# Kernel tuning notes

Hardware: AMD Instinct MI355X
Metric: run time of the kernel (lower is better)

The kernel has to match this reference:

```python
import jax, jax.numpy as jnp
import numpy as np

N = 50000
E = 800000
IN = 128
HID = 64
HEADS = 4
OUT = 128
NEG_SLOPE = 0.2


def _segment_softmax(logits, seg, num_segments):
    # logits: (E, H), seg: (E,) destination node ids
    m = jax.ops.segment_max(logits, seg, num_segments=num_segments)
    m = jnp.where(jnp.isfinite(m), m, 0.0)
    e = jnp.exp(logits - m[seg])
    s = jax.ops.segment_sum(e, seg, num_segments=num_segments)
    return e / (s[seg] + 1e-16)


def _gat_conv(x, edge_index, W, att_src, att_dst, bias, heads, out_ch, concat):
    # PyG GATConv with add_self_loops=True, negative_slope=0.2 (eval mode: no dropout)
    n = x.shape[0]
    loops = jnp.arange(n, dtype=edge_index.dtype)
    src = jnp.concatenate([edge_index[0], loops])
    dst = jnp.concatenate([edge_index[1], loops])
    h = (x @ W).reshape(n, heads, out_ch)                      # (N, H, C)
    a_src = jnp.einsum('nhc,hc->nh', h, att_src)               # (N, H)
    a_dst = jnp.einsum('nhc,hc->nh', h, att_dst)
    logits = jax.nn.leaky_relu(a_src[src] + a_dst[dst], NEG_SLOPE)  # (E', H)
    alpha = _segment_softmax(logits, dst, n)                   # (E', H)
    msg = alpha[:, :, None] * h[src]                           # (E', H, C)
    out = jax.ops.segment_sum(msg, dst, num_segments=n)        # (N, H, C)
    if concat:
        out = out.reshape(n, heads * out_ch)
    else:
        out = out.mean(axis=1)
    return out + bias


def setup_inputs() -> dict:
    key = jax.random.key(0)
    ks = jax.random.split(key, 16)
    hc = HID * HEADS
    s = 0.1
    return {
        'x': jax.random.normal(ks[0], (N, IN), dtype=jnp.float32),
        'edge_index': jax.random.randint(ks[1], (2, E), 0, N, dtype=jnp.int64),
        'W1': jax.random.normal(ks[2], (IN, hc), dtype=jnp.float32) * s,
        'att_src1': jax.random.normal(ks[3], (HEADS, HID), dtype=jnp.float32) * s,
        'att_dst1': jax.random.normal(ks[4], (HEADS, HID), dtype=jnp.float32) * s,
        'b1': jnp.zeros((hc,), dtype=jnp.float32),
        'lin1_w': jax.random.normal(ks[5], (IN, hc), dtype=jnp.float32) * s,
        'lin1_b': jnp.zeros((hc,), dtype=jnp.float32),
        'W2': jax.random.normal(ks[6], (hc, OUT), dtype=jnp.float32) * s,
        'att_src2': jax.random.normal(ks[7], (1, OUT), dtype=jnp.float32) * s,
        'att_dst2': jax.random.normal(ks[8], (1, OUT), dtype=jnp.float32) * s,
        'b2': jnp.zeros((OUT,), dtype=jnp.float32),
        'lin2_w': jax.random.normal(ks[9], (hc, OUT), dtype=jnp.float32) * s,
        'lin2_b': jnp.zeros((OUT,), dtype=jnp.float32),
    }


def reference(x, edge_index, W1, att_src1, att_dst1, b1, lin1_w, lin1_b,
              W2, att_src2, att_dst2, b2, lin2_w, lin2_b):
    # h1 = ELU(GATConv1(x) + Linear1(x))  (dropout is eval-mode no-op)
    h = _gat_conv(x, edge_index, W1, att_src1, att_dst1, b1, HEADS, HID, True)
    h = jax.nn.elu(h + x @ lin1_w + lin1_b)
    # out = GATConv2(h) + Linear2(h)
    o = _gat_conv(h, edge_index, W2, att_src2, att_dst2, b2, 1, OUT, False)
    return o + h @ lin2_w + lin2_b
```

## Files before the change

kernel.cpp:

```cpp
#include <hip/hip_runtime.h>
#include <math.h>

#define N_NODES 50000
#define N_EDGES 800000
#define EP (N_EDGES + N_NODES)
#define IN_CH 128
#define HID 64
#define HEADS 4
#define HC (HID * HEADS)
#define OUT_CH 128
#define NEG_SLOPE 0.2f
#define NSCAN ((N_NODES + 255) / 256)
#define MTILES (N_NODES / 16)

typedef __bf16 bf16x8 __attribute__((ext_vector_type(8)));
typedef float  f32x4  __attribute__((ext_vector_type(4)));

__device__ __forceinline__ float bf2f(unsigned short u) {
    return __uint_as_float(((unsigned)u) << 16);
}
__device__ __forceinline__ unsigned short f2bf(float f) {
    unsigned u = __float_as_uint(f);
    return (unsigned short)((u + 0x7fffu + ((u >> 16) & 1u)) >> 16);
}
__device__ __forceinline__ float lrelu(float v) {
    return v > 0.f ? v : NEG_SLOPE * v;
}
__device__ __forceinline__ bf16x8 ldfrag(const unsigned short* p) {
    uint4 u = *(const uint4*)p;
    return __builtin_bit_cast(bf16x8, u);
}

__global__ void hist_kernel(const int* __restrict__ ei, int* __restrict__ cnt) {
    int e = blockIdx.x * 256 + threadIdx.x;
    if (e >= EP) return;
    int d = (e < N_EDGES) ? ei[N_EDGES + e] : e - N_EDGES;
    atomicAdd(&cnt[d], 1);
}

__global__ void scan1_kernel(const int* __restrict__ cnt,
                             int* __restrict__ row, int* __restrict__ bsum) {
    __shared__ int buf[256];
    int i = blockIdx.x * 256 + threadIdx.x;
    int v = (i < N_NODES) ? cnt[i] : 0;
    buf[threadIdx.x] = v;
    __syncthreads();
#pragma unroll
    for (int off = 1; off < 256; off <<= 1) {
        int t = (threadIdx.x >= off) ? buf[threadIdx.x - off] : 0;
        __syncthreads();
        buf[threadIdx.x] += t;
        __syncthreads();
    }
    if (i < N_NODES) row[i] = buf[threadIdx.x] - v;
    if (threadIdx.x == 255) bsum[blockIdx.x] = buf[255];
}

__global__ void scan2_kernel(const int* __restrict__ bsum,
                             int* __restrict__ boff, int* __restrict__ rowN) {
    __shared__ int buf[256];
    int tid = threadIdx.x;
    int v = (tid < NSCAN) ? bsum[tid] : 0;
    buf[tid] = v;
    __syncthreads();
#pragma unroll
    for (int off = 1; off < 256; off <<= 1) {
        int t = (tid >= off) ? buf[tid - off] : 0;
        __syncthreads();
        buf[tid] += t;
        __syncthreads();
    }
    if (tid < NSCAN) boff[tid] = buf[tid] - v;
    if (tid == 255) rowN[0] = buf[255];
}

__global__ void scan3_kernel(int* __restrict__ row, const int* __restrict__ boff,
                             int* __restrict__ pos) {
    int i = blockIdx.x * 256 + threadIdx.x;
    if (i >= N_NODES) return;
    int r = row[i] + boff[blockIdx.x];
    row[i] = r;
    pos[i] = r;
}

__global__ void scatter_kernel(const int* __restrict__ ei,
                               int* __restrict__ pos,
                               int* __restrict__ adjS, int* __restrict__ adjD) {
    int e = blockIdx.x * 256 + threadIdx.x;
    if (e >= EP) return;
    int s, d;
    if (e < N_EDGES) { s = ei[e]; d = ei[N_EDGES + e]; }
    else             { s = d = e - N_EDGES; }
    int p = atomicAdd(&pos[d], 1);
    adjS[p] = s;
    adjD[p] = d;
}

__global__ void convx_kernel(const float* __restrict__ x,
                             unsigned short* __restrict__ xb) {
    int i = blockIdx.x * 256 + threadIdx.x;
    if (i >= N_NODES * (IN_CH / 4)) return;
    float4 v = ((const float4*)x)[i];
    ushort4 o;
    o.x = f2bf(v.x); o.y = f2bf(v.y); o.z = f2bf(v.z); o.w = f2bf(v.w);
    ((ushort4*)xb)[i] = o;
}

__global__ void pack1_kernel(const float* __restrict__ W1,
                             const float* __restrict__ L1,
                             unsigned short* __restrict__ Bp) {
    int t = blockIdx.x * 256 + threadIdx.x;
    if (t >= 128 * 64) return;
    int frag = t >> 6, l = t & 63;
    int ks = frag >> 5, nf = frag & 31;
    int col = nf * 16 + (l & 15);
    int kb = ks * 32 + (l >> 4) * 8;
    unsigned short* o = Bp + (size_t)t * 8;
#pragma unroll
    for (int i = 0; i < 8; ++i) {
        int k = kb + i;
        float v = (col < HC) ? W1[k * HC + col] : L1[k * HC + (col - HC)];
        o[i] = f2bf(v);
    }
}

__global__ void pack2_kernel(const float* __restrict__ W2,
                             const float* __restrict__ L2,
                             unsigned short* __restrict__ Bp) {
    int t = blockIdx.x * 256 + threadIdx.x;
    if (t >= 128 * 64) return;
    int frag = t >> 6, l = t & 63;
    int ks = frag >> 4, nf = frag & 15;
    int col = nf * 16 + (l & 15);
    int kb = ks * 32 + (l >> 4) * 8;
    unsigned short* o = Bp + (size_t)t * 8;
#pragma unroll
    for (int i = 0; i < 8; ++i) {
        int k = kb + i;
        float v = (col < OUT_CH) ? W2[k * OUT_CH + col]
                                 : L2[k * OUT_CH + (col - OUT_CH)];
        o[i] = f2bf(v);
    }
}

__global__ __launch_bounds__(256) void gemm1_mfma(
        const unsigned short* __restrict__ xb,
        const unsigned short* __restrict__ Bp,
        unsigned short* __restrict__ H1b, float* __restrict__ XL1) {
    int m0 = blockIdx.x * 16;
    int w = threadIdx.x >> 6, l = threadIdx.x & 63;
    int row = m0 + (l & 15);
    int koff = (l >> 4) * 8;
    f32x4 acc[8];
#pragma unroll
    for (int f = 0; f < 8; ++f) acc[f] = (f32x4){0.f, 0.f, 0.f, 0.f};
#pragma unroll
    for (int ks = 0; ks < 4; ++ks) {
        bf16x8 a = ldfrag(xb + (size_t)row * IN_CH + ks * 32 + koff);
        const unsigned short* bb = Bp + ((size_t)((ks * 32 + w * 8) * 64 + l)) * 8;
#pragma unroll
        for (int f = 0; f < 8; ++f) {
            bf16x8 b = ldfrag(bb + (size_t)f * 512);
            acc[f] = __builtin_amdgcn_mfma_f32_16x16x32_bf16(a, b, acc[f], 0, 0, 0);
        }
    }
    int rq = (l >> 4) * 4, lc = l & 15;
#pragma unroll
    for (int f = 0; f < 8; ++f) {
        int col = w * 128 + f * 16 + lc;
#pragma unroll
        for (int r = 0; r < 4; ++r) {
            int m = m0 + rq + r;
            float v = acc[f][r];
            if (col < HC) H1b[(size_t)m * HC + col] = f2bf(v);
            else          XL1[(size_t)m * HC + (col - HC)] = v;
        }
    }
}

__global__ __launch_bounds__(256) void gemm2_mfma(
        const unsigned short* __restrict__ HBb,
        const unsigned short* __restrict__ Bp,
        unsigned short* __restrict__ H2b, float* __restrict__ XL2) {
    int m0 = blockIdx.x * 16;
    int w = threadIdx.x >> 6, l = threadIdx.x & 63;
    int row = m0 + (l & 15);
    int koff = (l >> 4) * 8;
    f32x4 acc[4];
#pragma unroll
    for (int f = 0; f < 4; ++f) acc[f] = (f32x4){0.f, 0.f, 0.f, 0.f};
#pragma unroll
    for (int ks = 0; ks < 8; ++ks) {
        bf16x8 a = ldfrag(HBb + (size_t)row * HC + ks * 32 + koff);
        const unsigned short* bb = Bp + ((size_t)((ks * 16 + w * 4) * 64 + l)) * 8;
#pragma unroll
        for (int f = 0; f < 4; ++f) {
            bf16x8 b = ldfrag(bb + (size_t)f * 512);
            acc[f] = __builtin_amdgcn_mfma_f32_16x16x32_bf16(a, b, acc[f], 0, 0, 0);
        }
    }
    int rq = (l >> 4) * 4, lc = l & 15;
#pragma unroll
    for (int f = 0; f < 4; ++f) {
        int col = w * 64 + f * 16 + lc;
#pragma unroll
        for (int r = 0; r < 4; ++r) {
            int m = m0 + rq + r;
            float v = acc[f][r];
            if (col < OUT_CH) H2b[(size_t)m * OUT_CH + col] = f2bf(v);
            else              XL2[(size_t)m * OUT_CH + (col - OUT_CH)] = v;
        }
    }
}

__global__ void att1_kernel(const unsigned short* __restrict__ H1b,
                            const float* __restrict__ as,
                            const float* __restrict__ ad,
                            float* __restrict__ AS, float* __restrict__ AD) {
    int n = blockIdx.x * 4 + (threadIdx.x >> 6);
    int l = threadIdx.x & 63;
    if (n >= N_NODES) return;
    const unsigned short* h = H1b + (size_t)n * HC;
    float vs[HEADS], vd[HEADS];
#pragma unroll
    for (int hh = 0; hh < HEADS; ++hh) {
        float v = bf2f(h[hh * HID + l]);
        vs[hh] = v * as[hh * HID + l];
        vd[hh] = v * ad[hh * HID + l];
    }
#pragma unroll
    for (int off = 32; off; off >>= 1)
#pragma unroll
        for (int hh = 0; hh < HEADS; ++hh) {
            vs[hh] += __shfl_down(vs[hh], off, 64);
            vd[hh] += __shfl_down(vd[hh], off, 64);
        }
    if (l == 0)
#pragma unroll
        for (int hh = 0; hh < HEADS; ++hh) {
            AS[n * HEADS + hh] = vs[hh];
            AD[n * HEADS + hh] = vd[hh];
        }
}

__global__ void att2_kernel(const unsigned short* __restrict__ H2b,
                            const float* __restrict__ as2,
                            const float* __restrict__ ad2,
                            float* __restrict__ AS, float* __restrict__ AD) {
    int n = blockIdx.x * 4 + (threadIdx.x >> 6);
    int l = threadIdx.x & 63;
    if (n >= N_NODES) return;
    const unsigned short* h = H2b + (size_t)n * OUT_CH;
    float v0 = bf2f(h[l]), v1 = bf2f(h[64 + l]);
    float vs = v0 * as2[l] + v1 * as2[64 + l];
    float vd = v0 * ad2[l] + v1 * ad2[64 + l];
#pragma unroll
    for (int off = 32; off; off >>= 1) {
        vs += __shfl_down(vs, off, 64);
        vd += __shfl_down(vd, off, 64);
    }
    if (l == 0) { AS[n] = vs; AD[n] = vd; }
}

__global__ void el1_kernel(const int* __restrict__ adjS,
                           const int* __restrict__ adjD,
                           const float* __restrict__ AS,
                           const float* __restrict__ AD,
                           float* __restrict__ EL) {
    int idx = blockIdx.x * 256 + threadIdx.x;
    if (idx >= HEADS * EP) return;
    int h = idx / EP, p = idx - h * EP;
    int s = adjS[p], d = adjD[p];
    EL[idx] = expf(lrelu(AS[s * HEADS + h] + AD[d * HEADS + h]));
}

__global__ void el2_kernel(const int* __restrict__ adjS,
                           const int* __restrict__ adjD,
                           const float* __restrict__ AS,
                           const float* __restrict__ AD,
                           float* __restrict__ EL) {
    int p = blockIdx.x * 256 + threadIdx.x;
    if (p >= EP) return;
    EL[p] = expf(lrelu(AS[adjS[p]] + AD[adjD[p]]));
}

__global__ void gather1_kernel(const int* __restrict__ row,
                               const int* __restrict__ adjS,
                               const float* __restrict__ EL,
                               const unsigned short* __restrict__ H1b,
                               const float* __restrict__ XL1,
                               const float* __restrict__ b1,
                               const float* __restrict__ l1b,
                               unsigned short* __restrict__ HBb) {
    int d = blockIdx.x, j = threadIdx.x;
    int hh = j >> 4;
    int beg = row[d], end = row[d + 1];
    const float* ELh = EL + (size_t)hh * EP;
    const ushort4* Hr = (const ushort4*)H1b;
    float a0 = 0.f, a1 = 0.f, a2 = 0.f, a3 = 0.f, esum = 0.f;
    int i = beg;
    for (; i + 4 <= end; i += 4) {
        int s0 = adjS[i], s1 = adjS[i + 1], s2 = adjS[i + 2], s3 = adjS[i + 3];
        float e0 = ELh[i], e1 = ELh[i + 1], e2 = ELh[i + 2], e3 = ELh[i + 3];
        ushort4 q0 = Hr[(size_t)s0 * 64 + j];
        ushort4 q1 = Hr[(size_t)s1 * 64 + j];
        ushort4 q2 = Hr[(size_t)s2 * 64 + j];
        ushort4 q3 = Hr[(size_t)s3 * 64 + j];
        a0 += e0 * bf2f(q0.x) + e1 * bf2f(q1.x) + e2 * bf2f(q2.x) + e3 * bf2f(q3.x);
        a1 += e0 * bf2f(q0.y) + e1 * bf2f(q1.y) + e2 * bf2f(q2.y) + e3 * bf2f(q3.y);
        a2 += e0 * bf2f(q0.z) + e1 * bf2f(q1.z) + e2 * bf2f(q2.z) + e3 * bf2f(q3.z);
        a3 += e0 * bf2f(q0.w) + e1 * bf2f(q1.w) + e2 * bf2f(q2.w) + e3 * bf2f(q3.w);
        esum += e0 + e1 + e2 + e3;
    }
    for (; i < end; ++i) {
        int s = adjS[i];
        float e = ELh[i];
        ushort4 q = Hr[(size_t)s * 64 + j];
        a0 += e * bf2f(q.x); a1 += e * bf2f(q.y);
        a2 += e * bf2f(q.z); a3 += e * bf2f(q.w);
        esum += e;
    }
    float inv = 1.f / (esum + 1e-16f);
    float4 xl = ((const float4*)XL1)[(size_t)d * 64 + j];
    float4 bb = ((const float4*)b1)[j];
    float4 lb = ((const float4*)l1b)[j];
    float v0 = a0 * inv + xl.x + bb.x + lb.x;
    float v1 = a1 * inv + xl.y + bb.y + lb.y;
    float v2 = a2 * inv + xl.z + bb.z + lb.z;
    float v3 = a3 * inv + xl.w + bb.w + lb.w;
    v0 = v0 > 0.f ? v0 : expm1f(v0);
    v1 = v1 > 0.f ? v1 : expm1f(v1);
    v2 = v2 > 0.f ? v2 : expm1f(v2);
    v3 = v3 > 0.f ? v3 : expm1f(v3);
    ushort4 o;
    o.x = f2bf(v0); o.y = f2bf(v1); o.z = f2bf(v2); o.w = f2bf(v3);
    ((ushort4*)HBb)[(size_t)d * 64 + j] = o;
}

__global__ void gather2_kernel(const int* __restrict__ row,
                               const int* __restrict__ adjS,
                               const float* __restrict__ EL,
                               const unsigned short* __restrict__ H2b,
                               const float* __restrict__ XL2,
                               const float* __restrict__ b2,
                               const float* __restrict__ l2b,
                               float* __restrict__ out) {
    int d = blockIdx.x, l = threadIdx.x;
    int beg = row[d], end = row[d + 1];
    const ushort2* Hr = (const ushort2*)H2b;
    float ax = 0.f, ay = 0.f, esum = 0.f;
    int i = beg;
    for (; i + 4 <= end; i += 4) {
        int s0 = adjS[i], s1 = adjS[i + 1], s2 = adjS[i + 2], s3 = adjS[i + 3];
        float e0 = EL[i], e1 = EL[i + 1], e2 = EL[i + 2], e3 = EL[i + 3];
        ushort2 q0 = Hr[(size_t)s0 * 64 + l];
        ushort2 q1 = Hr[(size_t)s1 * 64 + l];
        ushort2 q2 = Hr[(size_t)s2 * 64 + l];
        ushort2 q3 = Hr[(size_t)s3 * 64 + l];
        ax += e0 * bf2f(q0.x) + e1 * bf2f(q1.x) + e2 * bf2f(q2.x) + e3 * bf2f(q3.x);
        ay += e0 * bf2f(q0.y) + e1 * bf2f(q1.y) + e2 * bf2f(q2.y) + e3 * bf2f(q3.y);
        esum += e0 + e1 + e2 + e3;
    }
    for (; i < end; ++i) {
        int s = adjS[i];
        float e = EL[i];
        ushort2 q = Hr[(size_t)s * 64 + l];
        ax += e * bf2f(q.x); ay += e * bf2f(q.y);
        esum += e;
    }
    float inv = 1.f / (esum + 1e-16f);
    float2 xl = ((const float2*)XL2)[(size_t)d * 64 + l];
    float2 bb = ((const float2*)b2)[l];
    float2 lb = ((const float2*)l2b)[l];
    ((float2*)out)[(size_t)d * 64 + l] =
        make_float2(ax * inv + xl.x + bb.x + lb.x,
                    ay * inv + xl.y + bb.y + lb.y);
}

extern "C" void kernel_launch(void* const* d_in, const int* in_sizes, int n_in,
                              void* d_out, int out_size, void* d_ws, size_t ws_size,
                              hipStream_t stream) {
    const float* x    = (const float*)d_in[0];
    const int*   ei   = (const int*)d_in[1];
    const float* W1   = (const float*)d_in[2];
    const float* as1  = (const float*)d_in[3];
    const float* ad1  = (const float*)d_in[4];
    const float* b1   = (const float*)d_in[5];
    const float* l1w  = (const float*)d_in[6];
    const float* l1b  = (const float*)d_in[7];
    const float* W2   = (const float*)d_in[8];
    const float* as2  = (const float*)d_in[9];
    const float* ad2  = (const float*)d_in[10];
    const float* b2   = (const float*)d_in[11];
    const float* l2w  = (const float*)d_in[12];
    const float* l2b  = (const float*)d_in[13];
    float* out = (float*)d_out;

    float* ws = (float*)d_ws;
    unsigned short* xb  = (unsigned short*)ws;
    float* fp = ws + (size_t)N_NODES * 64;
    unsigned short* H1b = (unsigned short*)fp;
    fp += (size_t)N_NODES * 128;
    float* XL1 = fp;
    fp += (size_t)N_NODES * HC;
    unsigned short* HBb = (unsigned short*)fp;
    fp += (size_t)N_NODES * 128;
    float* AS1 = fp; fp += (size_t)N_NODES * HEADS;
    float* AD1 = fp; fp += (size_t)N_NODES * HEADS;
    float* AS2 = fp; fp += N_NODES;
    float* AD2 = fp; fp += N_NODES;
    float* EL1 = fp; fp += (size_t)HEADS * EP;
    unsigned short* Bp1 = (unsigned short*)fp; fp += 32768;
    unsigned short* Bp2 = (unsigned short*)fp; fp += 32768;
    int* cnt  = (int*)fp;
    int* row  = cnt + N_NODES;
    int* pos  = row + N_NODES + 1;
    int* bsum = pos + N_NODES;
    int* boff = bsum + NSCAN;
    int* adjS = boff + NSCAN;
    int* adjD = adjS + EP;
    unsigned short* H2b = H1b;
    float* XL2 = XL1;
    float* EL2 = EL1;

    int nE = (EP + 255) / 256;

    hipMemsetAsync(cnt, 0, N_NODES * 4, stream);
    hist_kernel<<<nE, 256, 0, stream>>>(ei, cnt);
    scan1_kernel<<<NSCAN, 256, 0, stream>>>(cnt, row, bsum);
    scan2_kernel<<<1, 256, 0, stream>>>(bsum, boff, row + N_NODES);
    scan3_kernel<<<NSCAN, 256, 0, stream>>>(row, boff, pos);
    scatter_kernel<<<nE, 256, 0, stream>>>(ei, pos, adjS, adjD);

    convx_kernel<<<(N_NODES * (IN_CH / 4) + 255) / 256, 256, 0, stream>>>(x, xb);
    pack1_kernel<<<(128 * 64 + 255) / 256, 256, 0, stream>>>(W1, l1w, Bp1);
    pack2_kernel<<<(128 * 64 + 255) / 256, 256, 0, stream>>>(W2, l2w, Bp2);

    gemm1_mfma<<<MTILES, 256, 0, stream>>>(xb, Bp1, H1b, XL1);
    att1_kernel<<<(N_NODES + 3) / 4, 256, 0, stream>>>(H1b, as1, ad1, AS1, AD1);
    el1_kernel<<<(HEADS * EP + 255) / 256, 256, 0, stream>>>(adjS, adjD, AS1, AD1, EL1);
    gather1_kernel<<<N_NODES, 64, 0, stream>>>(row, adjS, EL1, H1b, XL1,
                                               b1, l1b, HBb);

    gemm2_mfma<<<MTILES, 256, 0, stream>>>(HBb, Bp2, H2b, XL2);
    att2_kernel<<<(N_NODES + 3) / 4, 256, 0, stream>>>(H2b, as2, ad2, AS2, AD2);
    el2_kernel<<<nE, 256, 0, stream>>>(adjS, adjD, AS2, AD2, EL2);
    gather2_kernel<<<N_NODES, 64, 0, stream>>>(row, adjS, EL2, H2b, XL2,
                                               b2, l2b, out);
}
```

Before: 333.9 us.

## Fuse attention scores into GEMMs, merge edge-logit with CSR scatter, bf16 skip path

Attention-score dot products are now computed in the MFMA GEMM epilogues, which removes the separate att1/att2 kernels and their re-read of H. Layer-1 edge exponentials are computed inside the CSR scatter kernel and stored as float4 per edge position, replacing the el1 kernel and its head-major array. The two weight-pack kernels are merged into one. The linear skip outputs are stored as bf16 instead of fp32. The gather loops are unrolled to 8 edges with loads batched ahead of use. Together these cut kernel launches and memory traffic, but the skip path loses precision and the scatter kernel now does more work.

```diff
diff --git a/kernel.cpp b/kernel.cpp
--- a/kernel.cpp
+++ b/kernel.cpp
@@ -83,9 +83,12 @@
     pos[i] = r;
 }
 
-__global__ void scatter_kernel(const int* __restrict__ ei,
-                               int* __restrict__ pos,
-                               int* __restrict__ adjS, int* __restrict__ adjD) {
+__global__ void scatter_el1_kernel(const int* __restrict__ ei,
+                                   int* __restrict__ pos,
+                                   const float4* __restrict__ AS4,
+                                   const float4* __restrict__ AD4,
+                                   int* __restrict__ adjS, int* __restrict__ adjD,
+                                   float4* __restrict__ EL4) {
     int e = blockIdx.x * 256 + threadIdx.x;
     if (e >= EP) return;
     int s, d;
@@ -94,6 +97,13 @@
     int p = atomicAdd(&pos[d], 1);
     adjS[p] = s;
     adjD[p] = d;
+    float4 a = AS4[s], b = AD4[d];
+    float4 o;
+    o.x = expf(lrelu(a.x + b.x));
+    o.y = expf(lrelu(a.y + b.y));
+    o.z = expf(lrelu(a.z + b.z));
+    o.w = expf(lrelu(a.w + b.w));
+    EL4[p] = o;
 }
 
 __global__ void convx_kernel(const float* __restrict__ x,
@@ -106,57 +116,59 @@
     ((ushort4*)xb)[i] = o;
 }
 
-__global__ void pack1_kernel(const float* __restrict__ W1,
-                             const float* __restrict__ L1,
-                             unsigned short* __restrict__ Bp) {
+__global__ void pack12_kernel(const float* __restrict__ W1,
+                              const float* __restrict__ L1,
+                              const float* __restrict__ W2,
+                              const float* __restrict__ L2,
+                              unsigned short* __restrict__ Bp1,
+                              unsigned short* __restrict__ Bp2) {
     int t = blockIdx.x * 256 + threadIdx.x;
-    if (t >= 128 * 64) return;
-    int frag = t >> 6, l = t & 63;
-    int ks = frag >> 5, nf = frag & 31;
-    int col = nf * 16 + (l & 15);
-    int kb = ks * 32 + (l >> 4) * 8;
-    unsigned short* o = Bp + (size_t)t * 8;
-#pragma unroll
-    for (int i = 0; i < 8; ++i) {
-        int k = kb + i;
-        float v = (col < HC) ? W1[k * HC + col] : L1[k * HC + (col - HC)];
-        o[i] = f2bf(v);
-    }
-}
-
-__global__ void pack2_kernel(const float* __restrict__ W2,
-                             const float* __restrict__ L2,
-                             unsigned short* __restrict__ Bp) {
-    int t = blockIdx.x * 256 + threadIdx.x;
-    if (t >= 128 * 64) return;
-    int frag = t >> 6, l = t & 63;
-    int ks = frag >> 4, nf = frag & 15;
-    int col = nf * 16 + (l & 15);
-    int kb = ks * 32 + (l >> 4) * 8;
-    unsigned short* o = Bp + (size_t)t * 8;
-#pragma unroll
-    for (int i = 0; i < 8; ++i) {
-        int k = kb + i;
-        float v = (col < OUT_CH) ? W2[k * OUT_CH + col]
-                                 : L2[k * OUT_CH + (col - OUT_CH)];
-        o[i] = f2bf(v);
+    if (t < 8192) {
+        int frag = t >> 6, l = t & 63;
+        int ks = frag >> 5, nf = frag & 31;
+        int col = nf * 16 + (l & 15);
+        int kb = ks * 32 + (l >> 4) * 8;
+        unsigned short* o = Bp1 + (size_t)t * 8;
+#pragma unroll
+        for (int i = 0; i < 8; ++i) {
+            int k = kb + i;
+            float v = (col < HC) ? W1[k * HC + col] : L1[k * HC + (col - HC)];
+            o[i] = f2bf(v);
+        }
+    } else if (t < 16384) {
+        int u = t - 8192;
+        int frag = u >> 6, l = u & 63;
+        int ks = frag >> 4, nf = frag & 15;
+        int col = nf * 16 + (l & 15);
+        int kb = ks * 32 + (l >> 4) * 8;
+        unsigned short* o = Bp2 + (size_t)u * 8;
+#pragma unroll
+        for (int i = 0; i < 8; ++i) {
+            int k = kb + i;
+            float v = (col < OUT_CH) ? W2[k * OUT_CH + col]
+                                     : L2[k * OUT_CH + (col - OUT_CH)];
+            o[i] = f2bf(v);
+        }
     }
 }
 
 __global__ __launch_bounds__(256) void gemm1_mfma(
         const unsigned short* __restrict__ xb,
         const unsigned short* __restrict__ Bp,
-        unsigned short* __restrict__ H1b, float* __restrict__ XL1) {
+        const float* __restrict__ as1, const float* __restrict__ ad1,
+        unsigned short* __restrict__ H1b, unsigned short* __restrict__ XLb,
+        float* __restrict__ AS, float* __restrict__ AD) {
+    __shared__ float sAS[16][4], sAD[16][4];
     int m0 = blockIdx.x * 16;
     int w = threadIdx.x >> 6, l = threadIdx.x & 63;
-    int row = m0 + (l & 15);
+    int arow = m0 + (l & 15);
     int koff = (l >> 4) * 8;
     f32x4 acc[8];
 #pragma unroll
     for (int f = 0; f < 8; ++f) acc[f] = (f32x4){0.f, 0.f, 0.f, 0.f};
 #pragma unroll
     for (int ks = 0; ks < 4; ++ks) {
-        bf16x8 a = ldfrag(xb + (size_t)row * IN_CH + ks * 32 + koff);
+        bf16x8 a = ldfrag(xb + (size_t)arow * IN_CH + ks * 32 + koff);
         const unsigned short* bb = Bp + ((size_t)((ks * 32 + w * 8) * 64 + l)) * 8;
 #pragma unroll
         for (int f = 0; f < 8; ++f) {
@@ -164,34 +176,75 @@
             acc[f] = __builtin_amdgcn_mfma_f32_16x16x32_bf16(a, b, acc[f], 0, 0, 0);
         }
     }
-    int rq = (l >> 4) * 4, lc = l & 15;
+    int g = l >> 4, lc = l & 15;
 #pragma unroll
     for (int f = 0; f < 8; ++f) {
         int col = w * 128 + f * 16 + lc;
 #pragma unroll
         for (int r = 0; r < 4; ++r) {
-            int m = m0 + rq + r;
+            int m = m0 + g * 4 + r;
             float v = acc[f][r];
             if (col < HC) H1b[(size_t)m * HC + col] = f2bf(v);
-            else          XL1[(size_t)m * HC + (col - HC)] = v;
-        }
-    }
+            else          XLb[(size_t)m * HC + (col - HC)] = f2bf(v);
+        }
+    }
+    if (w < 2) {
+        float ps[4][2], pd[4][2];
+#pragma unroll
+        for (int r = 0; r < 4; ++r) { ps[r][0]=ps[r][1]=pd[r][0]=pd[r][1]=0.f; }
+#pragma unroll
+        for (int f = 0; f < 8; ++f) {
+            int col = w * 128 + f * 16 + lc;
+            float av = as1[col], dv = ad1[col];
+            int hp = f >> 2;
+#pragma unroll
+            for (int r = 0; r < 4; ++r) {
+                ps[r][hp] += acc[f][r] * av;
+                pd[r][hp] += acc[f][r] * dv;
+            }
+        }
+#pragma unroll
+        for (int msk = 1; msk < 16; msk <<= 1)
+#pragma unroll
+            for (int r = 0; r < 4; ++r) {
+                ps[r][0] += __shfl_xor(ps[r][0], msk, 64);
+                ps[r][1] += __shfl_xor(ps[r][1], msk, 64);
+                pd[r][0] += __shfl_xor(pd[r][0], msk, 64);
+                pd[r][1] += __shfl_xor(pd[r][1], msk, 64);
+            }
+        if (lc == 0)
+#pragma unroll
+            for (int r = 0; r < 4; ++r) {
+                sAS[g * 4 + r][w * 2 + 0] = ps[r][0];
+                sAS[g * 4 + r][w * 2 + 1] = ps[r][1];
+                sAD[g * 4 + r][w * 2 + 0] = pd[r][0];
+                sAD[g * 4 + r][w * 2 + 1] = pd[r][1];
+            }
+    }
+    __syncthreads();
+    int t = threadIdx.x;
+    if (t < 64)       AS[(m0 + (t >> 2)) * 4 + (t & 3)] = sAS[t >> 2][t & 3];
+    else if (t < 128) { int u = t - 64;
+                        AD[(m0 + (u >> 2)) * 4 + (u & 3)] = sAD[u >> 2][u & 3]; }
 }
 
 __global__ __launch_bounds__(256) void gemm2_mfma(
         const unsigned short* __restrict__ HBb,
         const unsigned short* __restrict__ Bp,
-        unsigned short* __restrict__ H2b, float* __restrict__ XL2) {
+        const float* __restrict__ as2, const float* __restrict__ ad2,
+        unsigned short* __restrict__ H2b, unsigned short* __restrict__ XLb,
+        float* __restrict__ AS, float* __restrict__ AD) {
+    __shared__ float sAS[16][2], sAD[16][2];
     int m0 = blockIdx.x * 16;
     int w = threadIdx.x >> 6, l = threadIdx.x & 63;
-    int row = m0 + (l & 15);
+    int arow = m0 + (l & 15);
     int koff = (l >> 4) * 8;
     f32x4 acc[4];
 #pragma unroll
     for (int f = 0; f < 4; ++f) acc[f] = (f32x4){0.f, 0.f, 0.f, 0.f};
 #pragma unroll
     for (int ks = 0; ks < 8; ++ks) {
-        bf16x8 a = ldfrag(HBb + (size_t)row * HC + ks * 32 + koff);
+        bf16x8 a = ldfrag(HBb + (size_t)arow * HC + ks * 32 + koff);
         const unsigned short* bb = Bp + ((size_t)((ks * 16 + w * 4) * 64 + l)) * 8;
 #pragma unroll
         for (int f = 0; f < 4; ++f) {
@@ -199,79 +252,50 @@
             acc[f] = __builtin_amdgcn_mfma_f32_16x16x32_bf16(a, b, acc[f], 0, 0, 0);
         }
     }
-    int rq = (l >> 4) * 4, lc = l & 15;
+    int g = l >> 4, lc = l & 15;
 #pragma unroll
     for (int f = 0; f < 4; ++f) {
         int col = w * 64 + f * 16 + lc;
 #pragma unroll
         for (int r = 0; r < 4; ++r) {
-            int m = m0 + rq + r;
+            int m = m0 + g * 4 + r;
             float v = acc[f][r];
             if (col < OUT_CH) H2b[(size_t)m * OUT_CH + col] = f2bf(v);
-            else              XL2[(size_t)m * OUT_CH + (col - OUT_CH)] = v;
-        }
-    }
-}
-
-__global__ void att1_kernel(const unsigned short* __restrict__ H1b,
-                            const float* __restrict__ as,
-                            const float* __restrict__ ad,
-                            float* __restrict__ AS, float* __restrict__ AD) {
-    int n = blockIdx.x * 4 + (threadIdx.x >> 6);
-    int l = threadIdx.x & 63;
-    if (n >= N_NODES) return;
-    const unsigned short* h = H1b + (size_t)n * HC;
-    float vs[HEADS], vd[HEADS];
-#pragma unroll
-    for (int hh = 0; hh < HEADS; ++hh) {
-        float v = bf2f(h[hh * HID + l]);
-        vs[hh] = v * as[hh * HID + l];
-        vd[hh] = v * ad[hh * HID + l];
-    }
-#pragma unroll
-    for (int off = 32; off; off >>= 1)
-#pragma unroll
-        for (int hh = 0; hh < HEADS; ++hh) {
-            vs[hh] += __shfl_down(vs[hh], off, 64);
-            vd[hh] += __shfl_down(vd[hh], off, 64);
-        }
-    if (l == 0)
-#pragma unroll
-        for (int hh = 0; hh < HEADS; ++hh) {
-            AS[n * HEADS + hh] = vs[hh];
-            AD[n * HEADS + hh] = vd[hh];
-        }
-}
-
-__global__ void att2_kernel(const unsigned short* __restrict__ H2b,
-                            const float* __restrict__ as2,
-                            const float* __restrict__ ad2,
-                            float* __restrict__ AS, float* __restrict__ AD) {
-    int n = blockIdx.x * 4 + (threadIdx.x >> 6);
-    int l = threadIdx.x & 63;
-    if (n >= N_NODES) return;
-    const unsigned short* h = H2b + (size_t)n * OUT_CH;
-    float v0 = bf2f(h[l]), v1 = bf2f(h[64 + l]);
-    float vs = v0 * as2[l] + v1 * as2[64 + l];
-    float vd = v0 * ad2[l] + v1 * ad2[64 + l];
-#pragma unroll
-    for (int off = 32; off; off >>= 1) {
-        vs += __shfl_down(vs, off, 64);
-        vd += __shfl_down(vd, off, 64);
-    }
-    if (l == 0) { AS[n] = vs; AD[n] = vd; }
-}
-
-__global__ void el1_kernel(const int* __restrict__ adjS,
-                           const int* __restrict__ adjD,
-                           const float* __restrict__ AS,
-                           const float* __restrict__ AD,
-                           float* __restrict__ EL) {
-    int idx = blockIdx.x * 256 + threadIdx.x;
-    if (idx >= HEADS * EP) return;
-    int h = idx / EP, p = idx - h * EP;
-    int s = adjS[p], d = adjD[p];
-    EL[idx] = expf(lrelu(AS[s * HEADS + h] + AD[d * HEADS + h]));
+            else              XLb[(size_t)m * OUT_CH + (col - OUT_CH)] = f2bf(v);
+        }
+    }
+    if (w < 2) {
+        float ps[4], pd[4];
+#pragma unroll
+        for (int r = 0; r < 4; ++r) { ps[r] = 0.f; pd[r] = 0.f; }
+#pragma unroll
+        for (int f = 0; f < 4; ++f) {
+            int col = w * 64 + f * 16 + lc;
+            float av = as2[col], dv = ad2[col];
+#pragma unroll
+            for (int r = 0; r < 4; ++r) {
+                ps[r] += acc[f][r] * av;
+                pd[r] += acc[f][r] * dv;
+            }
+        }
+#pragma unroll
+        for (int msk = 1; msk < 16; msk <<= 1)
+#pragma unroll
+            for (int r = 0; r < 4; ++r) {
+                ps[r] += __shfl_xor(ps[r], msk, 64);
+                pd[r] += __shfl_xor(pd[r], msk, 64);
+            }
+        if (lc == 0)
+#pragma unroll
+            for (int r = 0; r < 4; ++r) {
+                sAS[g * 4 + r][w] = ps[r];
+                sAD[g * 4 + r][w] = pd[r];
+            }
+    }
+    __syncthreads();
+    int t = threadIdx.x;
+    if (t < 16)       AS[m0 + t] = sAS[t][0] + sAS[t][1];
+    else if (t < 32)  { int u = t - 16; AD[m0 + u] = sAD[u][0] + sAD[u][1]; }
 }
 
 __global__ void el2_kernel(const int* __restrict__ adjS,
@@ -286,48 +310,53 @@
 
 __global__ void gather1_kernel(const int* __restrict__ row,
                                const int* __restrict__ adjS,
-                               const float* __restrict__ EL,
+                               const float4* __restrict__ EL4,
                                const unsigned short* __restrict__ H1b,
-                               const float* __restrict__ XL1,
+                               const unsigned short* __restrict__ XLb,
                                const float* __restrict__ b1,
                                const float* __restrict__ l1b,
                                unsigned short* __restrict__ HBb) {
     int d = blockIdx.x, j = threadIdx.x;
     int hh = j >> 4;
     int beg = row[d], end = row[d + 1];
-    const float* ELh = EL + (size_t)hh * EP;
     const ushort4* Hr = (const ushort4*)H1b;
     float a0 = 0.f, a1 = 0.f, a2 = 0.f, a3 = 0.f, esum = 0.f;
     int i = beg;
-    for (; i + 4 <= end; i += 4) {
-        int s0 = adjS[i], s1 = adjS[i + 1], s2 = adjS[i + 2], s3 = adjS[i + 3];
-        float e0 = ELh[i], e1 = ELh[i + 1], e2 = ELh[i + 2], e3 = ELh[i + 3];
-        ushort4 q0 = Hr[(size_t)s0 * 64 + j];
-        ushort4 q1 = Hr[(size_t)s1 * 64 + j];
-        ushort4 q2 = Hr[(size_t)s2 * 64 + j];
-        ushort4 q3 = Hr[(size_t)s3 * 64 + j];
-        a0 += e0 * bf2f(q0.x) + e1 * bf2f(q1.x) + e2 * bf2f(q2.x) + e3 * bf2f(q3.x);
-        a1 += e0 * bf2f(q0.y) + e1 * bf2f(q1.y) + e2 * bf2f(q2.y) + e3 * bf2f(q3.y);
-        a2 += e0 * bf2f(q0.z) + e1 * bf2f(q1.z) + e2 * bf2f(q2.z) + e3 * bf2f(q3.z);
-        a3 += e0 * bf2f(q0.w) + e1 * bf2f(q1.w) + e2 * bf2f(q2.w) + e3 * bf2f(q3.w);
-        esum += e0 + e1 + e2 + e3;
+    for (; i + 8 <= end; i += 8) {
+        int sa[8]; float ea[8]; ushort4 qa[8];
+#pragma unroll
+        for (int k = 0; k < 8; ++k) sa[k] = adjS[i + k];
+#pragma unroll
+        for (int k = 0; k < 8; ++k) {
+            float4 t = EL4[i + k];
+            ea[k] = hh < 2 ? (hh == 0 ? t.x : t.y) : (hh == 2 ? t.z : t.w);
+        }
+#pragma unroll
+        for (int k = 0; k < 8; ++k) qa[k] = Hr[(size_t)sa[k] * 64 + j];
+#pragma unroll
+        for (int k = 0; k < 8; ++k) {
+            a0 += ea[k] * bf2f(qa[k].x); a1 += ea[k] * bf2f(qa[k].y);
+            a2 += ea[k] * bf2f(qa[k].z); a3 += ea[k] * bf2f(qa[k].w);
+            esum += ea[k];
+        }
     }
     for (; i < end; ++i) {
         int s = adjS[i];
-        float e = ELh[i];
+        float4 t = EL4[i];
+        float e = hh < 2 ? (hh == 0 ? t.x : t.y) : (hh == 2 ? t.z : t.w);
         ushort4 q = Hr[(size_t)s * 64 + j];
         a0 += e * bf2f(q.x); a1 += e * bf2f(q.y);
         a2 += e * bf2f(q.z); a3 += e * bf2f(q.w);
         esum += e;
     }
     float inv = 1.f / (esum + 1e-16f);
-    float4 xl = ((const float4*)XL1)[(size_t)d * 64 + j];
+    ushort4 xq = ((const ushort4*)XLb)[(size_t)d * 64 + j];
     float4 bb = ((const float4*)b1)[j];
     float4 lb = ((const float4*)l1b)[j];
-    float v0 = a0 * inv + xl.x + bb.x + lb.x;
-    float v1 = a1 * inv + xl.y + bb.y + lb.y;
-    float v2 = a2 * inv + xl.z + bb.z + lb.z;
-    float v3 = a3 * inv + xl.w + bb.w + lb.w;
+    float v0 = a0 * inv + bf2f(xq.x) + bb.x + lb.x;
+    float v1 = a1 * inv + bf2f(xq.y) + bb.y + lb.y;
+    float v2 = a2 * inv + bf2f(xq.z) + bb.z + lb.z;
+    float v3 = a3 * inv + bf2f(xq.w) + bb.w + lb.w;
     v0 = v0 > 0.f ? v0 : expm1f(v0);
     v1 = v1 > 0.f ? v1 : expm1f(v1);
     v2 = v2 > 0.f ? v2 : expm1f(v2);
@@ -341,7 +370,7 @@
                                const int* __restrict__ adjS,
                                const float* __restrict__ EL,
                                const unsigned short* __restrict__ H2b,
-                               const float* __restrict__ XL2,
+                               const unsigned short* __restrict__ XLb,
                                const float* __restrict__ b2,
                                const float* __restrict__ l2b,
                                float* __restrict__ out) {
@@ -350,16 +379,20 @@
     const ushort2* Hr = (const ushort2*)H2b;
     float ax = 0.f, ay = 0.f, esum = 0.f;
     int i = beg;
-    for (; i + 4 <= end; i += 4) {
-        int s0 = adjS[i], s1 = adjS[i + 1], s2 = adjS[i + 2], s3 = adjS[i + 3];
-        float e0 = EL[i], e1 = EL[i + 1], e2 = EL[i + 2], e3 = EL[i + 3];
-        ushort2 q0 = Hr[(size_t)s0 * 64 + l];
-        ushort2 q1 = Hr[(size_t)s1 * 64 + l];
-        ushort2 q2 = Hr[(size_t)s2 * 64 + l];
-        ushort2 q3 = Hr[(size_t)s3 * 64 + l];
-        ax += e0 * bf2f(q0.x) + e1 * bf2f(q1.x) + e2 * bf2f(q2.x) + e3 * bf2f(q3.x);
-        ay += e0 * bf2f(q0.y) + e1 * bf2f(q1.y) + e2 * bf2f(q2.y) + e3 * bf2f(q3.y);
-        esum += e0 + e1 + e2 + e3;
+    for (; i + 8 <= end; i += 8) {
+        int sa[8]; float ea[8]; ushort2 qa[8];
+#pragma unroll
+        for (int k = 0; k < 8; ++k) sa[k] = adjS[i + k];
+#pragma unroll
+        for (int k = 0; k < 8; ++k) ea[k] = EL[i + k];
+#pragma unroll
+        for (int k = 0; k < 8; ++k) qa[k] = Hr[(size_t)sa[k] * 64 + l];
+#pragma unroll
+        for (int k = 0; k < 8; ++k) {
+            ax += ea[k] * bf2f(qa[k].x);
+            ay += ea[k] * bf2f(qa[k].y);
+            esum += ea[k];
+        }
     }
     for (; i < end; ++i) {
         int s = adjS[i];
@@ -369,12 +402,12 @@
         esum += e;
     }
     float inv = 1.f / (esum + 1e-16f);
-    float2 xl = ((const float2*)XL2)[(size_t)d * 64 + l];
+    ushort2 xq = ((const ushort2*)XLb)[(size_t)d * 64 + l];
     float2 bb = ((const float2*)b2)[l];
     float2 lb = ((const float2*)l2b)[l];
     ((float2*)out)[(size_t)d * 64 + l] =
-        make_float2(ax * inv + xl.x + bb.x + lb.x,
-                    ay * inv + xl.y + bb.y + lb.y);
+        make_float2(ax * inv + bf2f(xq.x) + bb.x + lb.x,
+                    ay * inv + bf2f(xq.y) + bb.y + lb.y);
 }
 
 extern "C" void kernel_launch(void* const* d_in, const int* in_sizes, int n_in,
@@ -401,15 +434,15 @@
     float* fp = ws + (size_t)N_NODES * 64;
     unsigned short* H1b = (unsigned short*)fp;
     fp += (size_t)N_NODES * 128;
-    float* XL1 = fp;
-    fp += (size_t)N_NODES * HC;
+    unsigned short* XLb = (unsigned short*)fp;
+    fp += (size_t)N_NODES * 128;
     unsigned short* HBb = (unsigned short*)fp;
     fp += (size_t)N_NODES * 128;
     float* AS1 = fp; fp += (size_t)N_NODES * HEADS;
     float* AD1 = fp; fp += (size_t)N_NODES * HEADS;
     float* AS2 = fp; fp += N_NODES;
     float* AD2 = fp; fp += N_NODES;
-    float* EL1 = fp; fp += (size_t)HEADS * EP;
+    float* EL1 = fp; fp += (size_t)EP * 4;
     unsigned short* Bp1 = (unsigned short*)fp; fp += 32768;
     unsigned short* Bp2 = (unsigned short*)fp; fp += 32768;
     int* cnt  = (int*)fp;
@@ -420,7 +453,7 @@
     int* adjS = boff + NSCAN;
     int* adjD = adjS + EP;
     unsigned short* H2b = H1b;
-    float* XL2 = XL1;
+    unsigned short* XL2b = XLb;
     float* EL2 = EL1;
 
     int nE = (EP + 255) / 256;
@@ -430,21 +463,19 @@
     scan1_kernel<<<NSCAN, 256, 0, stream>>>(cnt, row, bsum);
     scan2_kernel<<<1, 256, 0, stream>>>(bsum, boff, row + N_NODES);
     scan3_kernel<<<NSCAN, 256, 0, stream>>>(row, boff, pos);
-    scatter_kernel<<<nE, 256, 0, stream>>>(ei, pos, adjS, adjD);
 
     convx_kernel<<<(N_NODES * (IN_CH / 4) + 255) / 256, 256, 0, stream>>>(x, xb);
-    pack1_kernel<<<(128 * 64 + 255) / 256, 256, 0, stream>>>(W1, l1w, Bp1);
-    pack2_kernel<<<(128 * 64 + 255) / 256, 256, 0, stream>>>(W2, l2w, Bp2);
-
-    gemm1_mfma<<<MTILES, 256, 0, stream>>>(xb, Bp1, H1b, XL1);
-    att1_kernel<<<(N_NODES + 3) / 4, 256, 0, stream>>>(H1b, as1, ad1, AS1, AD1);
-    el1_kernel<<<(HEADS * EP + 255) / 256, 256, 0, stream>>>(adjS, adjD, AS1, AD1, EL1);
-    gather1_kernel<<<N_NODES, 64, 0, stream>>>(row, adjS, EL1, H1b, XL1,
-                                               b1, l1b, HBb);
-
-    gemm2_mfma<<<MTILES, 256, 0, stream>>>(HBb, Bp2, H2b, XL2);
-    att2_kernel<<<(N_NODES + 3) / 4, 256, 0, stream>>>(H2b, as2, ad2, AS2, AD2);
+    pack12_kernel<<<64, 256, 0, stream>>>(W1, l1w, W2, l2w, Bp1, Bp2);
+
+    gemm1_mfma<<<MTILES, 256, 0, stream>>>(xb, Bp1, as1, ad1, H1b, XLb, AS1, AD1);
+    scatter_el1_kernel<<<nE, 256, 0, stream>>>(ei, pos, (const float4*)AS1,
+                                               (const float4*)AD1, adjS, adjD,
+                                               (float4*)EL1);
+    gather1_kernel<<<N_NODES, 64, 0, stream>>>(row, adjS, (const float4*)EL1,
+                                               H1b, XLb, b1, l1b, HBb);
+
+    gemm2_mfma<<<MTILES, 256, 0, stream>>>(HBb, Bp2, as2, ad2, H2b, XL2b, AS2, AD2);
     el2_kernel<<<nE, 256, 0, stream>>>(adjS, adjD, AS2, AD2, EL2);
-    gather2_kernel<<<N_NODES, 64, 0, stream>>>(row, adjS, EL2, H2b, XL2,
+    gather2_kernel<<<N_NODES, 64, 0, stream>>>(row, adjS, EL2, H2b, XL2b,
                                                b2, l2b, out);
 }
```

Result: faster. 280.0 us (-16.1%).
